# Performance work log

Measured on AMD Instinct MI355X. Metric: run time of the kernel, lower is better.

The kernel has to match this reference:

```python
import jax, jax.numpy as jnp
import numpy as np

B = 1024
D = 384  # inputdim


def setup_inputs() -> dict:
    key = jax.random.key(0)
    ks = jax.random.split(key, 6)
    s = 0.02
    return {
        "hspatial": jax.random.normal(ks[0], (B, D), dtype=jnp.float32),
        "htext": jax.random.normal(ks[1], (B, D), dtype=jnp.float32),
        "W_L": jax.random.normal(ks[2], (2 * D, 2 * D), dtype=jnp.float32) * s,
        "b_L": jax.random.normal(ks[3], (2 * D,), dtype=jnp.float32) * s,
        "W_L2": jax.random.normal(ks[4], (2 * D, D * D), dtype=jnp.float32) * s,
        "b_L2": jax.random.normal(ks[5], (2 * D,), dtype=jnp.float32) * s,
    }


def reference(hspatial, htext, W_L, b_L, W_L2, b_L2):
    # deep path: Linear on concatenated features -> [B, 2D]
    g = jnp.concatenate((hspatial, htext), axis=1) @ W_L.T + b_L
    # wide path: per-sample outer product flattened -> [B, D*D], then Linear
    # (vectorized replacement of the python per-sample loop)
    v = (hspatial[:, :, None] * htext[:, None, :]).reshape(hspatial.shape[0], -1)
    u = v @ W_L2.T + b_L2  # [B, 2D]
    return jnp.concatenate((g, u), axis=1)  # [B, 4D]
```

## Files before the change

kernel.cpp:

```cpp
#include <hip/hip_runtime.h>
#include <stdint.h>

typedef __attribute__((ext_vector_type(8))) __bf16 bf16x8;
typedef __attribute__((ext_vector_type(4))) float f32x4;

#define BATCH 1024
#define DDIM 384
#define NOUT 768
#define KWIDE (DDIM * DDIM)
#define KDEEP (2 * DDIM)
#define LDO (4 * DDIM)

#define BM 128
#define BN 128
#define BK 64
#define SPLITS 16

union P8 { __bf16 b[8]; uint4 u; };
union P4 { __bf16 b[4]; uint2 u; };

__device__ inline uint4 cvt8(float4 f0, float4 f1) {
    P8 p;
    p.b[0] = (__bf16)f0.x; p.b[1] = (__bf16)f0.y;
    p.b[2] = (__bf16)f0.z; p.b[3] = (__bf16)f0.w;
    p.b[4] = (__bf16)f1.x; p.b[5] = (__bf16)f1.y;
    p.b[6] = (__bf16)f1.z; p.b[7] = (__bf16)f1.w;
    return p.u;
}

__device__ inline uint4 cvt8s(float4 f0, float4 f1, float s) {
    P8 p;
    p.b[0] = (__bf16)(s * f0.x); p.b[1] = (__bf16)(s * f0.y);
    p.b[2] = (__bf16)(s * f0.z); p.b[3] = (__bf16)(s * f0.w);
    p.b[4] = (__bf16)(s * f1.x); p.b[5] = (__bf16)(s * f1.y);
    p.b[6] = (__bf16)(s * f1.z); p.b[7] = (__bf16)(s * f1.w);
    return p.u;
}

__global__ __launch_bounds__(256) void convert_weights(
    const float* __restrict__ w2, const float* __restrict__ wl,
    __bf16* __restrict__ o2, __bf16* __restrict__ ol) {
    const size_t n2 = (size_t)NOUT * KWIDE / 4;
    const size_t nl = (size_t)NOUT * KDEEP / 4;
    const size_t stride = (size_t)gridDim.x * blockDim.x;
    for (size_t v = (size_t)blockIdx.x * blockDim.x + threadIdx.x; v < n2; v += stride) {
        float4 f = ((const float4*)w2)[v];
        P4 p;
        p.b[0] = (__bf16)f.x; p.b[1] = (__bf16)f.y;
        p.b[2] = (__bf16)f.z; p.b[3] = (__bf16)f.w;
        ((uint2*)o2)[v] = p.u;
    }
    for (size_t v = (size_t)blockIdx.x * blockDim.x + threadIdx.x; v < nl; v += stride) {
        float4 f = ((const float4*)wl)[v];
        P4 p;
        p.b[0] = (__bf16)f.x; p.b[1] = (__bf16)f.y;
        p.b[2] = (__bf16)f.z; p.b[3] = (__bf16)f.w;
        ((uint2*)ol)[v] = p.u;
    }
}

__global__ __launch_bounds__(256) void init_bias(
    const float* __restrict__ bl, const float* __restrict__ bl2,
    float* __restrict__ out) {
    int idx = blockIdx.x * 256 + threadIdx.x;
    if (idx < BATCH * LDO) {
        int c = idx % LDO;
        out[idx] = (c < NOUT) ? bl[c] : bl2[c - NOUT];
    }
}

template <bool WBF16, bool WIDE>
__global__ __launch_bounds__(256) void gemm_fused(
    const float* __restrict__ hs, const float* __restrict__ ht,
    const void* __restrict__ wv, float* __restrict__ out,
    int Ktot, int kchunk, int coloff) {

    __shared__ __bf16 As[BM * BK];
    __shared__ __bf16 Bs[BN * BK];

    const int tid  = threadIdx.x;
    const int lane = tid & 63;
    const int wave = tid >> 6;
    const int quad = lane >> 4;
    const int lrow = lane & 15;
    const int wm   = (wave >> 1) * 64;
    const int wn   = (wave & 1) * 64;
    const int m0   = blockIdx.x * BM;
    const int n0   = blockIdx.y * BN;
    const int kb   = blockIdx.z * kchunk;
    const int ke   = kb + kchunk;

    const int ar = tid >> 3;
    const int ac = (tid & 7) * 8;

    f32x4 acc[4][4] = {};

    for (int k0 = kb; k0 < ke; k0 += BK) {
        if (WBF16) {
            const __bf16* w = (const __bf16*)wv;
#pragma unroll
            for (int q = 0; q < 4; ++q) {
                int r = ar + 32 * q;
                uint4 v = *(const uint4*)(w + (size_t)(n0 + r) * Ktot + k0 + ac);
                *(uint4*)&Bs[r * BK + ac] = v;
            }
        } else {
            const float* w = (const float*)wv;
#pragma unroll
            for (int q = 0; q < 4; ++q) {
                int r = ar + 32 * q;
                const float* src = w + (size_t)(n0 + r) * Ktot + k0 + ac;
                float4 f0 = *(const float4*)src;
                float4 f1 = *(const float4*)(src + 4);
                *(uint4*)&Bs[r * BK + ac] = cvt8(f0, f1);
            }
        }
        if (WIDE) {
            const int i  = k0 / DDIM;
            const int j0 = k0 % DDIM;
#pragma unroll
            for (int q = 0; q < 4; ++q) {
                int r = ar + 32 * q;
                float s = hs[(size_t)(m0 + r) * DDIM + i];
                const float* src = ht + (size_t)(m0 + r) * DDIM + j0 + ac;
                float4 f0 = *(const float4*)src;
                float4 f1 = *(const float4*)(src + 4);
                *(uint4*)&As[r * BK + ac] = cvt8s(f0, f1, s);
            }
        } else {
            int k = k0 + ac;
            const float* base = (k < DDIM) ? hs : ht;
            int kk = (k < DDIM) ? k : k - DDIM;
#pragma unroll
            for (int q = 0; q < 4; ++q) {
                int r = ar + 32 * q;
                const float* src = base + (size_t)(m0 + r) * DDIM + kk;
                float4 f0 = *(const float4*)src;
                float4 f1 = *(const float4*)(src + 4);
                *(uint4*)&As[r * BK + ac] = cvt8(f0, f1);
            }
        }
        __syncthreads();
#pragma unroll
        for (int s = 0; s < 2; ++s) {
            bf16x8 af[4], bfr[4];
#pragma unroll
            for (int t = 0; t < 4; ++t)
                af[t] = *(const bf16x8*)&As[(wm + t * 16 + lrow) * BK + s * 32 + quad * 8];
#pragma unroll
            for (int t = 0; t < 4; ++t)
                bfr[t] = *(const bf16x8*)&Bs[(wn + t * 16 + lrow) * BK + s * 32 + quad * 8];
#pragma unroll
            for (int i2 = 0; i2 < 4; ++i2)
#pragma unroll
                for (int j2 = 0; j2 < 4; ++j2)
                    acc[i2][j2] = __builtin_amdgcn_mfma_f32_16x16x32_bf16(
                        af[i2], bfr[j2], acc[i2][j2], 0, 0, 0);
        }
        __syncthreads();
    }

#pragma unroll
    for (int i2 = 0; i2 < 4; ++i2) {
#pragma unroll
        for (int j2 = 0; j2 < 4; ++j2) {
            int gr = m0 + wm + i2 * 16 + quad * 4;
            int gc = coloff + n0 + wn + j2 * 16 + lrow;
#pragma unroll
            for (int r = 0; r < 4; ++r)
                atomicAdd(&out[(size_t)(gr + r) * LDO + gc], acc[i2][j2][r]);
        }
    }
}

extern "C" void kernel_launch(void* const* d_in, const int* in_sizes, int n_in,
                              void* d_out, int out_size, void* d_ws, size_t ws_size,
                              hipStream_t stream) {
    const float* hs  = (const float*)d_in[0];
    const float* ht  = (const float*)d_in[1];
    const float* wl  = (const float*)d_in[2];
    const float* bl  = (const float*)d_in[3];
    const float* w2  = (const float*)d_in[4];
    const float* bl2 = (const float*)d_in[5];
    float* out = (float*)d_out;

    const size_t n2   = (size_t)NOUT * KWIDE;
    const size_t nl   = (size_t)NOUT * KDEEP;
    const size_t need = (n2 + nl) * 2;
    const bool bf16path = (ws_size >= need);

    dim3 blk(256);
    init_bias<<<(BATCH * LDO + 255) / 256, blk, 0, stream>>>(bl, bl2, out);

    if (bf16path) {
        __bf16* o2 = (__bf16*)d_ws;
        __bf16* ol = o2 + n2;
        convert_weights<<<4096, blk, 0, stream>>>(w2, wl, o2, ol);
        gemm_fused<true, false><<<dim3(8, 6, 1), blk, 0, stream>>>(
            hs, ht, (const void*)ol, out, KDEEP, KDEEP, 0);
        gemm_fused<true, true><<<dim3(8, 6, SPLITS), blk, 0, stream>>>(
            hs, ht, (const void*)o2, out, KWIDE, KWIDE / SPLITS, NOUT);
    } else {
        gemm_fused<false, false><<<dim3(8, 6, 1), blk, 0, stream>>>(
            hs, ht, (const void*)wl, out, KDEEP, KDEEP, 0);
        gemm_fused<false, true><<<dim3(8, 6, SPLITS), blk, 0, stream>>>(
            hs, ht, (const void*)w2, out, KWIDE, KWIDE / SPLITS, NOUT);
    }
}
```

Baseline: 1.268 ms.

## Drop bf16 weight preconversion, prefetch tiles into registers, pad LDS, double splits

Removes the separate kernel that converted the large fp32 wide weight matrix to bf16 in workspace, and instead converts fp32 weights on the fly inside the GEMM. Adds register-level prefetch of the next K tile during MFMA compute, pads the LDS row stride to cut bank conflicts, and raises split-K count to 32 for more parallel blocks. This avoids an extra full read and write of the weights, at the cost of reading fp32 weights (twice the bytes) in the GEMM, more registers, and more atomic adds.

```diff
diff --git a/kernel.cpp b/kernel.cpp
--- a/kernel.cpp
+++ b/kernel.cpp
@@ -14,10 +14,10 @@
 #define BM 128
 #define BN 128
 #define BK 64
-#define SPLITS 16
+#define LDSK 72
+#define SPLITS 32
 
 union P8 { __bf16 b[8]; uint4 u; };
-union P4 { __bf16 b[4]; uint2 u; };
 
 __device__ inline uint4 cvt8(float4 f0, float4 f1) {
     P8 p;
@@ -37,28 +37,6 @@
     return p.u;
 }
 
-__global__ __launch_bounds__(256) void convert_weights(
-    const float* __restrict__ w2, const float* __restrict__ wl,
-    __bf16* __restrict__ o2, __bf16* __restrict__ ol) {
-    const size_t n2 = (size_t)NOUT * KWIDE / 4;
-    const size_t nl = (size_t)NOUT * KDEEP / 4;
-    const size_t stride = (size_t)gridDim.x * blockDim.x;
-    for (size_t v = (size_t)blockIdx.x * blockDim.x + threadIdx.x; v < n2; v += stride) {
-        float4 f = ((const float4*)w2)[v];
-        P4 p;
-        p.b[0] = (__bf16)f.x; p.b[1] = (__bf16)f.y;
-        p.b[2] = (__bf16)f.z; p.b[3] = (__bf16)f.w;
-        ((uint2*)o2)[v] = p.u;
-    }
-    for (size_t v = (size_t)blockIdx.x * blockDim.x + threadIdx.x; v < nl; v += stride) {
-        float4 f = ((const float4*)wl)[v];
-        P4 p;
-        p.b[0] = (__bf16)f.x; p.b[1] = (__bf16)f.y;
-        p.b[2] = (__bf16)f.z; p.b[3] = (__bf16)f.w;
-        ((uint2*)ol)[v] = p.u;
-    }
-}
-
 __global__ __launch_bounds__(256) void init_bias(
     const float* __restrict__ bl, const float* __restrict__ bl2,
     float* __restrict__ out) {
@@ -69,14 +47,14 @@
     }
 }
 
-template <bool WBF16, bool WIDE>
+template <bool WIDE>
 __global__ __launch_bounds__(256) void gemm_fused(
     const float* __restrict__ hs, const float* __restrict__ ht,
-    const void* __restrict__ wv, float* __restrict__ out,
+    const float* __restrict__ w, float* __restrict__ out,
     int Ktot, int kchunk, int coloff) {
 
-    __shared__ __bf16 As[BM * BK];
-    __shared__ __bf16 Bs[BN * BK];
+    __shared__ __bf16 As[BM * LDSK];
+    __shared__ __bf16 Bs[BN * LDSK];
 
     const int tid  = threadIdx.x;
     const int lane = tid & 63;
@@ -95,37 +73,27 @@
 
     f32x4 acc[4][4] = {};
 
-    for (int k0 = kb; k0 < ke; k0 += BK) {
-        if (WBF16) {
-            const __bf16* w = (const __bf16*)wv;
+    float4 wb[4][2];
+    float4 ab[4][2];
+    float  sb[4];
+
+    auto load_tile = [&](int k0) {
 #pragma unroll
-            for (int q = 0; q < 4; ++q) {
-                int r = ar + 32 * q;
-                uint4 v = *(const uint4*)(w + (size_t)(n0 + r) * Ktot + k0 + ac);
-                *(uint4*)&Bs[r * BK + ac] = v;
-            }
-        } else {
-            const float* w = (const float*)wv;
-#pragma unroll
-            for (int q = 0; q < 4; ++q) {
-                int r = ar + 32 * q;
-                const float* src = w + (size_t)(n0 + r) * Ktot + k0 + ac;
-                float4 f0 = *(const float4*)src;
-                float4 f1 = *(const float4*)(src + 4);
-                *(uint4*)&Bs[r * BK + ac] = cvt8(f0, f1);
-            }
+        for (int q = 0; q < 4; ++q) {
+            const float* bsrc = w + (size_t)(n0 + ar + 32 * q) * Ktot + k0 + ac;
+            wb[q][0] = *(const float4*)bsrc;
+            wb[q][1] = *(const float4*)(bsrc + 4);
         }
         if (WIDE) {
             const int i  = k0 / DDIM;
             const int j0 = k0 % DDIM;
 #pragma unroll
             for (int q = 0; q < 4; ++q) {
-                int r = ar + 32 * q;
-                float s = hs[(size_t)(m0 + r) * DDIM + i];
-                const float* src = ht + (size_t)(m0 + r) * DDIM + j0 + ac;
-                float4 f0 = *(const float4*)src;
-                float4 f1 = *(const float4*)(src + 4);
-                *(uint4*)&As[r * BK + ac] = cvt8s(f0, f1, s);
+                const size_t r = (size_t)(m0 + ar + 32 * q) * DDIM;
+                sb[q] = hs[r + i];
+                const float* asrc = ht + r + j0 + ac;
+                ab[q][0] = *(const float4*)asrc;
+                ab[q][1] = *(const float4*)(asrc + 4);
             }
         } else {
             int k = k0 + ac;
@@ -133,23 +101,38 @@
             int kk = (k < DDIM) ? k : k - DDIM;
 #pragma unroll
             for (int q = 0; q < 4; ++q) {
-                int r = ar + 32 * q;
-                const float* src = base + (size_t)(m0 + r) * DDIM + kk;
-                float4 f0 = *(const float4*)src;
-                float4 f1 = *(const float4*)(src + 4);
-                *(uint4*)&As[r * BK + ac] = cvt8(f0, f1);
+                const float* asrc = base + (size_t)(m0 + ar + 32 * q) * DDIM + kk;
+                ab[q][0] = *(const float4*)asrc;
+                ab[q][1] = *(const float4*)(asrc + 4);
             }
         }
+    };
+
+    auto store_tile = [&]() {
+#pragma unroll
+        for (int q = 0; q < 4; ++q) {
+            int r = ar + 32 * q;
+            *(uint4*)&Bs[r * LDSK + ac] = cvt8(wb[q][0], wb[q][1]);
+            *(uint4*)&As[r * LDSK + ac] =
+                WIDE ? cvt8s(ab[q][0], ab[q][1], sb[q]) : cvt8(ab[q][0], ab[q][1]);
+        }
+    };
+
+    load_tile(kb);
+
+    for (int k0 = kb; k0 < ke; k0 += BK) {
+        store_tile();
         __syncthreads();
+        if (k0 + BK < ke) load_tile(k0 + BK);
 #pragma unroll
         for (int s = 0; s < 2; ++s) {
             bf16x8 af[4], bfr[4];
 #pragma unroll
             for (int t = 0; t < 4; ++t)
-                af[t] = *(const bf16x8*)&As[(wm + t * 16 + lrow) * BK + s * 32 + quad * 8];
+                af[t] = *(const bf16x8*)&As[(wm + t * 16 + lrow) * LDSK + s * 32 + quad * 8];
 #pragma unroll
             for (int t = 0; t < 4; ++t)
-                bfr[t] = *(const bf16x8*)&Bs[(wn + t * 16 + lrow) * BK + s * 32 + quad * 8];
+                bfr[t] = *(const bf16x8*)&Bs[(wn + t * 16 + lrow) * LDSK + s * 32 + quad * 8];
 #pragma unroll
             for (int i2 = 0; i2 < 4; ++i2)
 #pragma unroll
@@ -184,26 +167,11 @@
     const float* bl2 = (const float*)d_in[5];
     float* out = (float*)d_out;
 
-    const size_t n2   = (size_t)NOUT * KWIDE;
-    const size_t nl   = (size_t)NOUT * KDEEP;
-    const size_t need = (n2 + nl) * 2;
-    const bool bf16path = (ws_size >= need);
-
     dim3 blk(256);
     init_bias<<<(BATCH * LDO + 255) / 256, blk, 0, stream>>>(bl, bl2, out);
 
-    if (bf16path) {
-        __bf16* o2 = (__bf16*)d_ws;
-        __bf16* ol = o2 + n2;
-        convert_weights<<<4096, blk, 0, stream>>>(w2, wl, o2, ol);
-        gemm_fused<true, false><<<dim3(8, 6, 1), blk, 0, stream>>>(
-            hs, ht, (const void*)ol, out, KDEEP, KDEEP, 0);
-        gemm_fused<true, true><<<dim3(8, 6, SPLITS), blk, 0, stream>>>(
-            hs, ht, (const void*)o2, out, KWIDE, KWIDE / SPLITS, NOUT);
-    } else {
-        gemm_fused<false, false><<<dim3(8, 6, 1), blk, 0, stream>>>(
-            hs, ht, (const void*)wl, out, KDEEP, KDEEP, 0);
-        gemm_fused<false, true><<<dim3(8, 6, SPLITS), blk, 0, stream>>>(
-            hs, ht, (const void*)w2, out, KWIDE, KWIDE / SPLITS, NOUT);
-    }
+    gemm_fused<false><<<dim3(8, 6, 1), blk, 0, stream>>>(
+        hs, ht, wl, out, KDEEP, KDEEP, 0);
+    gemm_fused<true><<<dim3(8, 6, SPLITS), blk, 0, stream>>>(
+        hs, ht, w2, out, KWIDE, KWIDE / SPLITS, NOUT);
 }
```

Result: faster. 1.133 ms (-10.7%).
